# Optimization experiments

Hardware: AMD Instinct MI355X
Metric: run time of the kernel (lower is better)

The kernel has to match this reference:

```python
import jax, jax.numpy as jnp
import numpy as np

B, S, HID = 2, 2048, 3072
H, HKV, D = 16, 8, 256
ROPE_THETA = 10000.0
NEG_INF = -1e9


def setup_inputs() -> dict:
    key = jax.random.key(0)
    ks = jax.random.split(key, 5)
    hidden_states = jax.random.normal(ks[0], (B, S, HID), jnp.float32)
    # rotary frequencies: complex freqs_cis = cos + i*sin, shape (B, S, D//2)
    inv_freq = 1.0 / (ROPE_THETA ** (np.arange(0, D, 2, dtype=np.float32) / D))
    ang = np.arange(S, dtype=np.float32)[:, None] * inv_freq[None, :]  # (S, D//2)
    cos = jnp.asarray(np.broadcast_to(np.cos(ang)[None], (B, S, D // 2)).copy())
    sin = jnp.asarray(np.broadcast_to(np.sin(ang)[None], (B, S, D // 2)).copy())
    causal = jnp.tril(jnp.ones((S, S), dtype=bool))
    mask = jnp.where(causal, 0.0, NEG_INF).astype(jnp.float32)[None, None]  # (1,1,S,S)
    wq = jax.random.normal(ks[1], (HID, H * D), jnp.float32) * 0.02
    wk = jax.random.normal(ks[2], (HID, HKV * D), jnp.float32) * 0.02
    wv = jax.random.normal(ks[3], (HID, HKV * D), jnp.float32) * 0.02
    wo = jax.random.normal(ks[4], (H * D, HID), jnp.float32) * 0.02
    return {"hidden_states": hidden_states, "cos": cos, "sin": sin, "mask": mask,
            "wq": wq, "wk": wk, "wv": wv, "wo": wo}


def _apply_rotary(x, cos, sin):
    # x: (B, S, Hx, D). Torch code forms complex pairs (x[..., :D/2], x[..., D/2:])
    # and multiplies by freqs_cis = cos + i*sin, then re-concats real||imag halves.
    half = x.shape[-1] // 2
    x1, x2 = x[..., :half], x[..., half:]
    c = cos[:, :, None, :]  # (B, S, 1, D/2)
    s = sin[:, :, None, :]
    return jnp.concatenate([x1 * c - x2 * s, x1 * s + x2 * c], axis=-1)


def reference(hidden_states, cos, sin, mask, wq, wk, wv, wo):
    b, s, _ = hidden_states.shape
    q = (hidden_states @ wq).reshape(b, s, H, D)
    k = (hidden_states @ wk).reshape(b, s, HKV, D)
    v = (hidden_states @ wv).reshape(b, s, HKV, D)
    q = _apply_rotary(q, cos, sin)
    k = _apply_rotary(k, cos, sin)
    # GQA: group query heads per kv head instead of materializing repeated K/V
    g = H // HKV
    qg = q.reshape(b, s, HKV, g, D)
    scaling = D ** (-0.5)
    scores = jnp.einsum('bskgd,btkd->bkgst', qg, k) * scaling  # (B,HKV,G,S,S)
    scores = scores + mask[:, :, None]  # broadcast (1,1,1,S,S)
    probs = jax.nn.softmax(scores, axis=-1)
    out = jnp.einsum('bkgst,btkd->bskgd', probs, v).reshape(b, s, H * D)
    return out @ wo
```

## Files before the change

kernel.cpp:

```cpp
#include <hip/hip_runtime.h>

typedef short bf16x8 __attribute__((ext_vector_type(8)));
typedef float f32x4 __attribute__((ext_vector_type(4)));

#define S_LEN 2048
#define NHQ 16
#define NKV 8
#define HD 256

__device__ __forceinline__ unsigned short f2bf(float f){
  unsigned u = __float_as_uint(f);
  unsigned r = (u + 0x7FFFu + ((u >> 16) & 1u)) >> 16;
  return (unsigned short)r;
}
__device__ __forceinline__ float bf2f(unsigned short h){
  return __uint_as_float(((unsigned)h) << 16);
}
__device__ __forceinline__ unsigned pack2(float a, float b){
  return (unsigned)f2bf(a) | ((unsigned)f2bf(b) << 16);
}

__device__ __forceinline__ void gload_lds16(const void* g, void* l){
  __builtin_amdgcn_global_load_lds(
      (const __attribute__((address_space(1))) void*)g,
      (__attribute__((address_space(3))) void*)l, 16, 0, 0);
}

__global__ void k_conv(const float* __restrict__ in, unsigned short* __restrict__ out, int n){
  int i = (blockIdx.x * 256 + threadIdx.x) * 4;
  if (i < n){
    float4 v = *(const float4*)&in[i];
    ushort4 o;
    o.x = f2bf(v.x); o.y = f2bf(v.y); o.z = f2bf(v.z); o.w = f2bf(v.w);
    *(ushort4*)&out[i] = o;
  }
}

__global__ void k_tconv(const float* __restrict__ in, unsigned short* __restrict__ out, int R, int C){
  __shared__ float tile[32][33];
  int c0 = blockIdx.x * 32, r0 = blockIdx.y * 32;
  int tx = threadIdx.x, ty = threadIdx.y;
  for (int i = 0; i < 4; i++)
    tile[ty + i*8][tx] = in[(size_t)(r0 + ty + i*8) * C + c0 + tx];
  __syncthreads();
  for (int i = 0; i < 4; i++)
    out[(size_t)(c0 + ty + i*8) * R + r0 + tx] = f2bf(tile[tx][ty + i*8]);
}

__global__ void k_vtrans(const unsigned short* __restrict__ V, unsigned short* __restrict__ VT){
  __shared__ unsigned short tile[32][40];
  int s0 = blockIdx.x * 32, d0 = blockIdx.y * 32, bz = blockIdx.z;
  int b = bz >> 3, kv = bz & 7;
  int tx = threadIdx.x, ty = threadIdx.y;
  for (int i = 0; i < 4; i++)
    tile[ty + i*8][tx] = V[(size_t)(b * S_LEN + s0 + ty + i*8) * (NKV*HD) + kv*HD + d0 + tx];
  __syncthreads();
  for (int i = 0; i < 4; i++)
    VT[((size_t)(bz * HD + d0 + ty + i*8)) * S_LEN + s0 + tx] = tile[tx][ty + i*8];
}

__global__ void k_rope(unsigned short* buf, const float* __restrict__ cosb,
                       const float* __restrict__ sinb, int lgnh){
  int idx = blockIdx.x * 256 + threadIdx.x;
  int d0 = (idx & 15) * 8;
  int h = (idx >> 4) & ((1 << lgnh) - 1);
  int t = idx >> (4 + lgnh);
  float ca[8], sa[8];
  *(float4*)&ca[0] = *(const float4*)&cosb[t * 128 + d0];
  *(float4*)&ca[4] = *(const float4*)&cosb[t * 128 + d0 + 4];
  *(float4*)&sa[0] = *(const float4*)&sinb[t * 128 + d0];
  *(float4*)&sa[4] = *(const float4*)&sinb[t * 128 + d0 + 4];
  size_t base = ((size_t)t << (lgnh + 8)) + ((size_t)h << 8) + d0;
  bf16x8 x1 = *(const bf16x8*)&buf[base];
  bf16x8 x2 = *(const bf16x8*)&buf[base + 128];
  bf16x8 o1, o2;
  #pragma unroll
  for (int j = 0; j < 8; j++){
    float f1 = bf2f((unsigned short)x1[j]), f2 = bf2f((unsigned short)x2[j]);
    o1[j] = (short)f2bf(f1 * ca[j] - f2 * sa[j]);
    o2[j] = (short)f2bf(f1 * sa[j] + f2 * ca[j]);
  }
  *(bf16x8*)&buf[base] = o1;
  *(bf16x8*)&buf[base + 128] = o2;
}

__global__ __launch_bounds__(256) void k_gemm_bt(const unsigned short* __restrict__ A,
    const unsigned short* __restrict__ Bt, void* __restrict__ Cp,
    int M, int N, int K, int out_bf16){
  __shared__ __align__(16) unsigned short smem[2 * 128 * 64];
  unsigned short* As = smem;
  unsigned short* Bs = smem + 128 * 64;
  int tid = threadIdx.x;
  int lane = tid & 63, wave = tid >> 6, quad = lane >> 4, l16 = lane & 15;
  int wm = wave >> 1, wn = wave & 1;
  int nx = gridDim.x;
  int flat = blockIdx.y * nx + blockIdx.x;
  int cpx = (nx * gridDim.y) >> 3;
  int swz = (flat & 7) * cpx + (flat >> 3);
  int bm0 = (swz / nx) * 128, bn0 = (swz % nx) * 128;
  const unsigned short* Ag = &A[(size_t)bm0 * K];
  const unsigned short* Bg = &Bt[(size_t)bn0 * K];
  int srow = lane >> 3;
  int spc  = lane & 7;
  f32x4 acc[4][4] = {};
  for (int k0 = 0; k0 < K; k0 += 64){
    __syncthreads();
    for (int it = 0; it < 4; it++){
      int win = it * 4 + wave;
      int row = win * 8 + srow;
      int c   = spc ^ (row & 7);
      gload_lds16(&Ag[(size_t)row * K + k0 + c * 8], &As[win * 512]);
      gload_lds16(&Bg[(size_t)row * K + k0 + c * 8], &Bs[win * 512]);
    }
    __syncthreads();
    for (int ks = 0; ks < 2; ks++){
      bf16x8 af[4], bfr[4];
      for (int mt = 0; mt < 4; mt++){
        int row = wm * 64 + mt * 16 + l16;
        int pc = (ks * 4 + quad) ^ (row & 7);
        af[mt] = *(const bf16x8*)&As[row * 64 + pc * 8];
      }
      for (int nt = 0; nt < 4; nt++){
        int row = wn * 64 + nt * 16 + l16;
        int pc = (ks * 4 + quad) ^ (row & 7);
        bfr[nt] = *(const bf16x8*)&Bs[row * 64 + pc * 8];
      }
      for (int mt = 0; mt < 4; mt++)
        for (int nt = 0; nt < 4; nt++)
          acc[mt][nt] = __builtin_amdgcn_mfma_f32_16x16x32_bf16(af[mt], bfr[nt], acc[mt][nt], 0, 0, 0);
    }
  }
  float* Ct = (float*)smem;
  for (int p = 0; p < 2; p++){
    __syncthreads();
    if (wm == p){
      for (int mt = 0; mt < 4; mt++)
        for (int nt = 0; nt < 4; nt++)
          for (int r = 0; r < 4; r++)
            Ct[(mt * 16 + quad * 4 + r) * 128 + wn * 64 + nt * 16 + l16] = acc[mt][nt][r];
    }
    __syncthreads();
    if (out_bf16){
      unsigned short* O = (unsigned short*)Cp;
      for (int j = 0; j < 4; j++){
        int chunk = j * 256 + tid;
        int row = chunk >> 4, col = (chunk & 15) * 8;
        const float* src = &Ct[row * 128 + col];
        uint4 o;
        o.x = pack2(src[0], src[1]);
        o.y = pack2(src[2], src[3]);
        o.z = pack2(src[4], src[5]);
        o.w = pack2(src[6], src[7]);
        *(uint4*)&O[(size_t)(bm0 + p * 64 + row) * N + bn0 + col] = o;
      }
    } else {
      float* O = (float*)Cp;
      for (int j = 0; j < 8; j++){
        int chunk = j * 256 + tid;
        int row = chunk >> 5, col = (chunk & 31) * 4;
        *(float4*)&O[(size_t)(bm0 + p * 64 + row) * N + bn0 + col] = *(const float4*)&Ct[row * 128 + col];
      }
    }
  }
}

__global__ __launch_bounds__(512, 2) void k_flash(const unsigned short* __restrict__ Q,
    const unsigned short* __restrict__ Kg, const unsigned short* __restrict__ VTg,
    unsigned short* __restrict__ Og){
  __shared__ __align__(16) unsigned short smem[2 * 17408 + 8 * 16 * 40];
  const int BUFSZ = 17408;
  int tid = threadIdx.x;
  int lane = tid & 63, wave = tid >> 6, quad = lane >> 4, l16 = lane & 15;
  int hig = wave & 1, rowgrp = wave >> 1;
  int bkv = blockIdx.x, y = blockIdx.y;
  int qt = (y < 16) ? y : 47 - y;
  int b = bkv >> 3, kv = bkv & 7;
  int h = kv * 2 + hig;
  const float L2E = 1.4426950408889634f;
  const float scale = 0.0625f;

  size_t kgbase = (size_t)(b * S_LEN) * (NKV*HD) + (size_t)kv * HD;
  size_t vtbase = ((size_t)(b * NKV + kv) * HD) * S_LEN;
  unsigned short* Ps = smem + 2 * BUFSZ + wave * (16 * 40);

  int qmin = qt * 64 + rowgrp * 16;
  int nkt = qt * 2 + 2;

  bf16x8 qf[8];
  {
    size_t qoff = ((size_t)(b * S_LEN + qt * 64 + rowgrp * 16 + l16)) * (NHQ * HD) + (size_t)h * HD;
    for (int ks = 0; ks < 8; ks++)
      qf[ks] = *(const bf16x8*)&Q[qoff + ks * 32 + quad * 8];
  }
  f32x4 acc[16] = {};
  float mrow[4], lrow[4];
  for (int r = 0; r < 4; r++){ mrow[r] = -1e30f; lrow[r] = 0.f; }

  uint4 stk[2], stv[2];
  for (int it = 0; it < 2; it++){
    int slot = it * 512 + tid;
    int kr = slot >> 5, c = slot & 31;
    stk[it] = *(const uint4*)&Kg[kgbase + (size_t)kr * (NKV*HD) + c * 8];
    int dd = slot >> 2, c2 = slot & 3;
    stv[it] = *(const uint4*)&VTg[vtbase + (size_t)dd * S_LEN + c2 * 8];
  }

  for (int kt = 0; kt < nkt; kt++){
    unsigned short* Ks  = smem + (kt & 1) * BUFSZ;
    unsigned short* VTs = Ks + 8192;
    for (int it = 0; it < 2; it++){
      int slot = it * 512 + tid;
      int kr = slot >> 5, c = slot & 31;
      *(uint4*)&Ks[kr * 256 + (c ^ kr) * 8] = stk[it];
      int dd = slot >> 2, c2 = slot & 3;
      *(uint4*)&VTs[dd * 36 + c2 * 8] = stv[it];
    }
    if (kt + 1 < nkt){
      for (int it = 0; it < 2; it++){
        int slot = it * 512 + tid;
        int kr = slot >> 5, c = slot & 31;
        stk[it] = *(const uint4*)&Kg[kgbase + (size_t)((kt + 1) * 32 + kr) * (NKV*HD) + c * 8];
        int dd = slot >> 2, c2 = slot & 3;
        stv[it] = *(const uint4*)&VTg[vtbase + (size_t)dd * S_LEN + (kt + 1) * 32 + c2 * 8];
      }
    }
    __syncthreads();
    if (kt * 32 > qmin + 15) continue;

    f32x4 sv[2] = {};
    __builtin_amdgcn_s_setprio(1);
    for (int ks = 0; ks < 8; ks++){
      for (int nt = 0; nt < 2; nt++){
        int row = nt * 16 + l16;
        bf16x8 kf = *(const bf16x8*)&Ks[row * 256 + ((ks * 4 + quad) ^ row) * 8];
        sv[nt] = __builtin_amdgcn_mfma_f32_16x16x32_bf16(qf[ks], kf, sv[nt], 0, 0, 0);
      }
    }
    __builtin_amdgcn_s_setprio(0);
    float pv[2][4], tmax[4];
    for (int r = 0; r < 4; r++){
      int qr = qmin + quad * 4 + r;
      float mx = -1e30f;
      for (int nt = 0; nt < 2; nt++){
        int key = kt * 32 + nt * 16 + l16;
        float v = sv[nt][r] * scale;
        if (key > qr) v = -1e30f;
        pv[nt][r] = v;
        mx = fmaxf(mx, v);
      }
      tmax[r] = mx;
    }
    for (int off = 1; off < 16; off <<= 1)
      for (int r = 0; r < 4; r++)
        tmax[r] = fmaxf(tmax[r], __shfl_xor(tmax[r], off, 64));
    int grow = (tmax[0] > mrow[0]) | (tmax[1] > mrow[1]) |
               (tmax[2] > mrow[2]) | (tmax[3] > mrow[3]);
    if (grow){
      float alpha[4];
      for (int r = 0; r < 4; r++){
        float mn = fmaxf(mrow[r], tmax[r]);
        alpha[r] = exp2f((mrow[r] - mn) * L2E);
        mrow[r] = mn;
        lrow[r] *= alpha[r];
      }
      for (int i = 0; i < 16; i++)
        for (int r = 0; r < 4; r++) acc[i][r] *= alpha[r];
    }
    float pb[2][4], psum[4] = {0.f, 0.f, 0.f, 0.f};
    for (int nt = 0; nt < 2; nt++)
      for (int r = 0; r < 4; r++){
        float pe = exp2f((pv[nt][r] - mrow[r]) * L2E);
        pb[nt][r] = pe; psum[r] += pe;
      }
    for (int off = 1; off < 16; off <<= 1)
      for (int r = 0; r < 4; r++)
        psum[r] += __shfl_xor(psum[r], off, 64);
    for (int r = 0; r < 4; r++) lrow[r] += psum[r];
    for (int nt = 0; nt < 2; nt++)
      for (int r = 0; r < 4; r++)
        Ps[(quad * 4 + r) * 40 + nt * 16 + l16] = f2bf(pb[nt][r]);
    bf16x8 pa = *(const bf16x8*)&Ps[l16 * 40 + quad * 8];
    __builtin_amdgcn_s_setprio(1);
    for (int nt = 0; nt < 16; nt++){
      bf16x8 vf = *(const bf16x8*)&VTs[(nt * 16 + l16) * 36 + quad * 8];
      acc[nt] = __builtin_amdgcn_mfma_f32_16x16x32_bf16(pa, vf, acc[nt], 0, 0, 0);
    }
    __builtin_amdgcn_s_setprio(0);
  }
  float inv[4];
  for (int r = 0; r < 4; r++) inv[r] = 1.0f / lrow[r];
  __syncthreads();
  unsigned short* Ot = smem + wave * (16 * 256);
  for (int nt = 0; nt < 16; nt++)
    for (int r = 0; r < 4; r++)
      Ot[(quad * 4 + r) * 256 + nt * 16 + l16] = f2bf(acc[nt][r] * inv[r]);
  size_t obase = ((size_t)(b * S_LEN + qt * 64 + rowgrp * 16)) * (NHQ * HD) + (size_t)h * HD;
  for (int j = 0; j < 8; j++){
    int chunk = j * 64 + lane;
    int row = chunk >> 5, col = (chunk & 31) * 8;
    *(uint4*)&Og[obase + (size_t)row * (NHQ * HD) + col] = *(const uint4*)&Ot[row * 256 + col];
  }
}

extern "C" void kernel_launch(void* const* d_in, const int* in_sizes, int n_in,
                              void* d_out, int out_size, void* d_ws, size_t ws_size,
                              hipStream_t stream){
  const float* hid  = (const float*)d_in[0];
  const float* cosb = (const float*)d_in[1];
  const float* sinb = (const float*)d_in[2];
  const float* wq = (const float*)d_in[4];
  const float* wk = (const float*)d_in[5];
  const float* wv = (const float*)d_in[6];
  const float* wo = (const float*)d_in[7];

  char* ws = (char*)d_ws;
  size_t off = 0;
  auto alloc = [&](size_t bytes) -> void* {
    void* p = ws + off; off += (bytes + 255) & ~(size_t)255; return p;
  };
  unsigned short* Xbf = (unsigned short*)alloc(4096ull * 3072 * 2);
  unsigned short* WqT = (unsigned short*)alloc(4096ull * 3072 * 2);
  unsigned short* WkT = (unsigned short*)alloc(2048ull * 3072 * 2);
  unsigned short* WvT = (unsigned short*)alloc(2048ull * 3072 * 2);
  unsigned short* WoT = (unsigned short*)alloc(3072ull * 4096 * 2);
  unsigned short* Qb  = (unsigned short*)alloc(4096ull * 4096 * 2);
  unsigned short* Kb  = (unsigned short*)alloc(4096ull * 2048 * 2);
  unsigned short* Vb  = (unsigned short*)alloc(4096ull * 2048 * 2);
  unsigned short* VTb = (unsigned short*)alloc(4096ull * 2048 * 2);
  unsigned short* Ab  = (unsigned short*)alloc(4096ull * 4096 * 2);

  k_conv<<<12288, 256, 0, stream>>>(hid, Xbf, 4096 * 3072);
  k_tconv<<<dim3(128, 96), dim3(32, 8), 0, stream>>>(wq, WqT, 3072, 4096);
  k_tconv<<<dim3(64, 96),  dim3(32, 8), 0, stream>>>(wk, WkT, 3072, 2048);
  k_tconv<<<dim3(64, 96),  dim3(32, 8), 0, stream>>>(wv, WvT, 3072, 2048);
  k_tconv<<<dim3(96, 128), dim3(32, 8), 0, stream>>>(wo, WoT, 4096, 3072);
  k_gemm_bt<<<dim3(32, 32), 256, 0, stream>>>(Xbf, WqT, Qb, 4096, 4096, 3072, 1);
  k_gemm_bt<<<dim3(16, 32), 256, 0, stream>>>(Xbf, WkT, Kb, 4096, 2048, 3072, 1);
  k_gemm_bt<<<dim3(16, 32), 256, 0, stream>>>(Xbf, WvT, Vb, 4096, 2048, 3072, 1);
  k_rope<<<4096, 256, 0, stream>>>(Qb, cosb, sinb, 4);
  k_rope<<<2048, 256, 0, stream>>>(Kb, cosb, sinb, 3);
  k_vtrans<<<dim3(64, 8, 16), dim3(32, 8), 0, stream>>>(Vb, VTb);
  k_flash<<<dim3(16, 32), 512, 0, stream>>>(Qb, Kb, VTb, Ab);
  k_gemm_bt<<<dim3(24, 32), 256, 0, stream>>>(Ab, WoT, d_out, 4096, 3072, 4096, 0);
}
```

Measured before the change: 1.091 ms.

## Pair causal query tiles per flash block, pad LDS, vectorize transposes

The flash attention kernel now processes two query tiles per block (p and 31-p), so every block does an equal amount of causal work and the grid is halved. This is meant to remove load imbalance and tail effects from short and long causal tiles. The K tile drops its XOR swizzle in favour of a row stride padded to 264, and the V-transpose row stride goes from 36 to 40. The transpose and conversion kernels now write 4 elements per thread as ushort4 stores instead of scalar stores. The trade-offs are fewer blocks in flight (256 instead of 512), a larger LDS footprint and a possible change in LDS bank conflicts.

```diff
diff --git a/kernel.cpp b/kernel.cpp
--- a/kernel.cpp
+++ b/kernel.cpp
@@ -43,8 +43,14 @@
   for (int i = 0; i < 4; i++)
     tile[ty + i*8][tx] = in[(size_t)(r0 + ty + i*8) * C + c0 + tx];
   __syncthreads();
-  for (int i = 0; i < 4; i++)
-    out[(size_t)(c0 + ty + i*8) * R + r0 + tx] = f2bf(tile[tx][ty + i*8]);
+  int tid = ty * 32 + tx;
+  int oc = tid >> 3, og = tid & 7;
+  ushort4 u;
+  u.x = f2bf(tile[og*4 + 0][oc]);
+  u.y = f2bf(tile[og*4 + 1][oc]);
+  u.z = f2bf(tile[og*4 + 2][oc]);
+  u.w = f2bf(tile[og*4 + 3][oc]);
+  *(ushort4*)&out[(size_t)(c0 + oc) * R + r0 + og*4] = u;
 }
 
 __global__ void k_vtrans(const unsigned short* __restrict__ V, unsigned short* __restrict__ VT){
@@ -55,8 +61,14 @@
   for (int i = 0; i < 4; i++)
     tile[ty + i*8][tx] = V[(size_t)(b * S_LEN + s0 + ty + i*8) * (NKV*HD) + kv*HD + d0 + tx];
   __syncthreads();
-  for (int i = 0; i < 4; i++)
-    VT[((size_t)(bz * HD + d0 + ty + i*8)) * S_LEN + s0 + tx] = tile[tx][ty + i*8];
+  int tid = ty * 32 + tx;
+  int oc = tid >> 3, og = tid & 7;
+  ushort4 u;
+  u.x = tile[og*4 + 0][oc];
+  u.y = tile[og*4 + 1][oc];
+  u.z = tile[og*4 + 2][oc];
+  u.w = tile[og*4 + 3][oc];
+  *(ushort4*)&VT[((size_t)(bz * HD + d0 + oc)) * S_LEN + s0 + og*4] = u;
 }
 
 __global__ void k_rope(unsigned short* buf, const float* __restrict__ cosb,
@@ -167,13 +179,12 @@
 __global__ __launch_bounds__(512, 2) void k_flash(const unsigned short* __restrict__ Q,
     const unsigned short* __restrict__ Kg, const unsigned short* __restrict__ VTg,
     unsigned short* __restrict__ Og){
-  __shared__ __align__(16) unsigned short smem[2 * 17408 + 8 * 16 * 40];
-  const int BUFSZ = 17408;
+  __shared__ __align__(16) unsigned short smem[2 * (32*264 + 256*40) + 8 * 16 * 40];
+  const int BUFSZ = 32*264 + 256*40;
   int tid = threadIdx.x;
   int lane = tid & 63, wave = tid >> 6, quad = lane >> 4, l16 = lane & 15;
   int hig = wave & 1, rowgrp = wave >> 1;
-  int bkv = blockIdx.x, y = blockIdx.y;
-  int qt = (y < 16) ? y : 47 - y;
+  int bkv = blockIdx.x, p = blockIdx.y;
   int b = bkv >> 3, kv = bkv & 7;
   int h = kv * 2 + hig;
   const float L2E = 1.4426950408889634f;
@@ -183,122 +194,125 @@
   size_t vtbase = ((size_t)(b * NKV + kv) * HD) * S_LEN;
   unsigned short* Ps = smem + 2 * BUFSZ + wave * (16 * 40);
 
-  int qmin = qt * 64 + rowgrp * 16;
-  int nkt = qt * 2 + 2;
-
-  bf16x8 qf[8];
-  {
-    size_t qoff = ((size_t)(b * S_LEN + qt * 64 + rowgrp * 16 + l16)) * (NHQ * HD) + (size_t)h * HD;
-    for (int ks = 0; ks < 8; ks++)
-      qf[ks] = *(const bf16x8*)&Q[qoff + ks * 32 + quad * 8];
-  }
-  f32x4 acc[16] = {};
-  float mrow[4], lrow[4];
-  for (int r = 0; r < 4; r++){ mrow[r] = -1e30f; lrow[r] = 0.f; }
-
-  uint4 stk[2], stv[2];
-  for (int it = 0; it < 2; it++){
-    int slot = it * 512 + tid;
-    int kr = slot >> 5, c = slot & 31;
-    stk[it] = *(const uint4*)&Kg[kgbase + (size_t)kr * (NKV*HD) + c * 8];
-    int dd = slot >> 2, c2 = slot & 3;
-    stv[it] = *(const uint4*)&VTg[vtbase + (size_t)dd * S_LEN + c2 * 8];
-  }
-
-  for (int kt = 0; kt < nkt; kt++){
-    unsigned short* Ks  = smem + (kt & 1) * BUFSZ;
-    unsigned short* VTs = Ks + 8192;
+  for (int ph = 0; ph < 2; ph++){
+    int qt = ph ? (31 - p) : p;
+    int qmin = qt * 64 + rowgrp * 16;
+    int nkt = qt * 2 + 2;
+
+    bf16x8 qf[8];
+    {
+      size_t qoff = ((size_t)(b * S_LEN + qt * 64 + rowgrp * 16 + l16)) * (NHQ * HD) + (size_t)h * HD;
+      for (int ks = 0; ks < 8; ks++)
+        qf[ks] = *(const bf16x8*)&Q[qoff + ks * 32 + quad * 8];
+    }
+    f32x4 acc[16] = {};
+    float mrow[4], lrow[4];
+    for (int r = 0; r < 4; r++){ mrow[r] = -1e30f; lrow[r] = 0.f; }
+
+    uint4 stk[2], stv[2];
     for (int it = 0; it < 2; it++){
       int slot = it * 512 + tid;
       int kr = slot >> 5, c = slot & 31;
-      *(uint4*)&Ks[kr * 256 + (c ^ kr) * 8] = stk[it];
+      stk[it] = *(const uint4*)&Kg[kgbase + (size_t)(kr) * (NKV*HD) + c * 8];
       int dd = slot >> 2, c2 = slot & 3;
-      *(uint4*)&VTs[dd * 36 + c2 * 8] = stv[it];
-    }
-    if (kt + 1 < nkt){
+      stv[it] = *(const uint4*)&VTg[vtbase + (size_t)dd * S_LEN + c2 * 8];
+    }
+
+    for (int kt = 0; kt < nkt; kt++){
+      unsigned short* Ks  = smem + (kt & 1) * BUFSZ;
+      unsigned short* VTs = Ks + 32 * 264;
       for (int it = 0; it < 2; it++){
         int slot = it * 512 + tid;
         int kr = slot >> 5, c = slot & 31;
-        stk[it] = *(const uint4*)&Kg[kgbase + (size_t)((kt + 1) * 32 + kr) * (NKV*HD) + c * 8];
+        *(uint4*)&Ks[kr * 264 + c * 8] = stk[it];
         int dd = slot >> 2, c2 = slot & 3;
-        stv[it] = *(const uint4*)&VTg[vtbase + (size_t)dd * S_LEN + (kt + 1) * 32 + c2 * 8];
-      }
-    }
-    __syncthreads();
-    if (kt * 32 > qmin + 15) continue;
-
-    f32x4 sv[2] = {};
-    __builtin_amdgcn_s_setprio(1);
-    for (int ks = 0; ks < 8; ks++){
-      for (int nt = 0; nt < 2; nt++){
-        int row = nt * 16 + l16;
-        bf16x8 kf = *(const bf16x8*)&Ks[row * 256 + ((ks * 4 + quad) ^ row) * 8];
-        sv[nt] = __builtin_amdgcn_mfma_f32_16x16x32_bf16(qf[ks], kf, sv[nt], 0, 0, 0);
-      }
-    }
-    __builtin_amdgcn_s_setprio(0);
-    float pv[2][4], tmax[4];
-    for (int r = 0; r < 4; r++){
-      int qr = qmin + quad * 4 + r;
-      float mx = -1e30f;
-      for (int nt = 0; nt < 2; nt++){
-        int key = kt * 32 + nt * 16 + l16;
-        float v = sv[nt][r] * scale;
-        if (key > qr) v = -1e30f;
-        pv[nt][r] = v;
-        mx = fmaxf(mx, v);
-      }
-      tmax[r] = mx;
-    }
-    for (int off = 1; off < 16; off <<= 1)
+        *(uint4*)&VTs[dd * 40 + c2 * 8] = stv[it];
+      }
+      if (kt + 1 < nkt){
+        for (int it = 0; it < 2; it++){
+          int slot = it * 512 + tid;
+          int kr = slot >> 5, c = slot & 31;
+          stk[it] = *(const uint4*)&Kg[kgbase + (size_t)((kt + 1) * 32 + kr) * (NKV*HD) + c * 8];
+          int dd = slot >> 2, c2 = slot & 3;
+          stv[it] = *(const uint4*)&VTg[vtbase + (size_t)dd * S_LEN + (kt + 1) * 32 + c2 * 8];
+        }
+      }
+      __syncthreads();
+      if (kt * 32 > qmin + 15) continue;
+
+      f32x4 sv[2] = {};
+      __builtin_amdgcn_s_setprio(1);
+      for (int ks = 0; ks < 8; ks++){
+        for (int nt = 0; nt < 2; nt++){
+          bf16x8 kf = *(const bf16x8*)&Ks[(nt * 16 + l16) * 264 + ks * 32 + quad * 8];
+          sv[nt] = __builtin_amdgcn_mfma_f32_16x16x32_bf16(qf[ks], kf, sv[nt], 0, 0, 0);
+        }
+      }
+      __builtin_amdgcn_s_setprio(0);
+      float pv[2][4], tmax[4];
+      for (int r = 0; r < 4; r++){
+        int qr = qmin + quad * 4 + r;
+        float mx = -1e30f;
+        for (int nt = 0; nt < 2; nt++){
+          int key = kt * 32 + nt * 16 + l16;
+          float v = sv[nt][r] * scale;
+          if (key > qr) v = -1e30f;
+          pv[nt][r] = v;
+          mx = fmaxf(mx, v);
+        }
+        tmax[r] = mx;
+      }
+      for (int off = 1; off < 16; off <<= 1)
+        for (int r = 0; r < 4; r++)
+          tmax[r] = fmaxf(tmax[r], __shfl_xor(tmax[r], off, 64));
+      int grow = (tmax[0] > mrow[0]) | (tmax[1] > mrow[1]) |
+                 (tmax[2] > mrow[2]) | (tmax[3] > mrow[3]);
+      if (grow){
+        float alpha[4];
+        for (int r = 0; r < 4; r++){
+          float mn = fmaxf(mrow[r], tmax[r]);
+          alpha[r] = exp2f((mrow[r] - mn) * L2E);
+          mrow[r] = mn;
+          lrow[r] *= alpha[r];
+        }
+        for (int i = 0; i < 16; i++)
+          for (int r = 0; r < 4; r++) acc[i][r] *= alpha[r];
+      }
+      float pb[2][4], psum[4] = {0.f, 0.f, 0.f, 0.f};
+      for (int nt = 0; nt < 2; nt++)
+        for (int r = 0; r < 4; r++){
+          float pe = exp2f((pv[nt][r] - mrow[r]) * L2E);
+          pb[nt][r] = pe; psum[r] += pe;
+        }
+      for (int off = 1; off < 16; off <<= 1)
+        for (int r = 0; r < 4; r++)
+          psum[r] += __shfl_xor(psum[r], off, 64);
+      for (int r = 0; r < 4; r++) lrow[r] += psum[r];
+      for (int nt = 0; nt < 2; nt++)
+        for (int r = 0; r < 4; r++)
+          Ps[(quad * 4 + r) * 40 + nt * 16 + l16] = f2bf(pb[nt][r]);
+      bf16x8 pa = *(const bf16x8*)&Ps[l16 * 40 + quad * 8];
+      __builtin_amdgcn_s_setprio(1);
+      for (int nt = 0; nt < 16; nt++){
+        bf16x8 vf = *(const bf16x8*)&VTs[(nt * 16 + l16) * 40 + quad * 8];
+        acc[nt] = __builtin_amdgcn_mfma_f32_16x16x32_bf16(pa, vf, acc[nt], 0, 0, 0);
+      }
+      __builtin_amdgcn_s_setprio(0);
+    }
+    float inv[4];
+    for (int r = 0; r < 4; r++) inv[r] = 1.0f / lrow[r];
+    __syncthreads();
+    unsigned short* Ot = smem + wave * (16 * 256);
+    for (int nt = 0; nt < 16; nt++)
       for (int r = 0; r < 4; r++)
-        tmax[r] = fmaxf(tmax[r], __shfl_xor(tmax[r], off, 64));
-    int grow = (tmax[0] > mrow[0]) | (tmax[1] > mrow[1]) |
-               (tmax[2] > mrow[2]) | (tmax[3] > mrow[3]);
-    if (grow){
-      float alpha[4];
-      for (int r = 0; r < 4; r++){
-        float mn = fmaxf(mrow[r], tmax[r]);
-        alpha[r] = exp2f((mrow[r] - mn) * L2E);
-        mrow[r] = mn;
-        lrow[r] *= alpha[r];
-      }
-      for (int i = 0; i < 16; i++)
-        for (int r = 0; r < 4; r++) acc[i][r] *= alpha[r];
-    }
-    float pb[2][4], psum[4] = {0.f, 0.f, 0.f, 0.f};
-    for (int nt = 0; nt < 2; nt++)
-      for (int r = 0; r < 4; r++){
-        float pe = exp2f((pv[nt][r] - mrow[r]) * L2E);
-        pb[nt][r] = pe; psum[r] += pe;
-      }
-    for (int off = 1; off < 16; off <<= 1)
-      for (int r = 0; r < 4; r++)
-        psum[r] += __shfl_xor(psum[r], off, 64);
-    for (int r = 0; r < 4; r++) lrow[r] += psum[r];
-    for (int nt = 0; nt < 2; nt++)
-      for (int r = 0; r < 4; r++)
-        Ps[(quad * 4 + r) * 40 + nt * 16 + l16] = f2bf(pb[nt][r]);
-    bf16x8 pa = *(const bf16x8*)&Ps[l16 * 40 + quad * 8];
-    __builtin_amdgcn_s_setprio(1);
-    for (int nt = 0; nt < 16; nt++){
-      bf16x8 vf = *(const bf16x8*)&VTs[(nt * 16 + l16) * 36 + quad * 8];
-      acc[nt] = __builtin_amdgcn_mfma_f32_16x16x32_bf16(pa, vf, acc[nt], 0, 0, 0);
-    }
-    __builtin_amdgcn_s_setprio(0);
-  }
-  float inv[4];
-  for (int r = 0; r < 4; r++) inv[r] = 1.0f / lrow[r];
-  __syncthreads();
-  unsigned short* Ot = smem + wave * (16 * 256);
-  for (int nt = 0; nt < 16; nt++)
-    for (int r = 0; r < 4; r++)
-      Ot[(quad * 4 + r) * 256 + nt * 16 + l16] = f2bf(acc[nt][r] * inv[r]);
-  size_t obase = ((size_t)(b * S_LEN + qt * 64 + rowgrp * 16)) * (NHQ * HD) + (size_t)h * HD;
-  for (int j = 0; j < 8; j++){
-    int chunk = j * 64 + lane;
-    int row = chunk >> 5, col = (chunk & 31) * 8;
-    *(uint4*)&Og[obase + (size_t)row * (NHQ * HD) + col] = *(const uint4*)&Ot[row * 256 + col];
+        Ot[(quad * 4 + r) * 256 + nt * 16 + l16] = f2bf(acc[nt][r] * inv[r]);
+    size_t obase = ((size_t)(b * S_LEN + qt * 64 + rowgrp * 16)) * (NHQ * HD) + (size_t)h * HD;
+    for (int j = 0; j < 8; j++){
+      int chunk = j * 64 + lane;
+      int row = chunk >> 5, col = (chunk & 31) * 8;
+      *(uint4*)&Og[obase + (size_t)row * (NHQ * HD) + col] = *(const uint4*)&Ot[row * 256 + col];
+    }
+    __syncthreads();
   }
 }
 
@@ -340,6 +354,6 @@
   k_rope<<<4096, 256, 0, stream>>>(Qb, cosb, sinb, 4);
   k_rope<<<2048, 256, 0, stream>>>(Kb, cosb, sinb, 3);
   k_vtrans<<<dim3(64, 8, 16), dim3(32, 8), 0, stream>>>(Vb, VTb);
-  k_flash<<<dim3(16, 32), 512, 0, stream>>>(Qb, Kb, VTb, Ab);
+  k_flash<<<dim3(16, 16), 512, 0, stream>>>(Qb, Kb, VTb, Ab);
   k_gemm_bt<<<dim3(24, 32), 256, 0, stream>>>(Ab, WoT, d_out, 4096, 3072, 4096, 0);
 }
```

Result: faster. 881.0 us (-19.2%).
